# Performance work log

Measured on AMD Instinct MI355X. Metric: run time of the kernel, lower is better.

## Reference

```python
import jax, jax.numpy as jnp
import numpy as np

B, ARITY = 4096, 6
EMB = 100
NF = 200
FC = 1200
N_ROLES, N_VALUES = 5000, 50000
BN_EPS = 1e-5


def setup_inputs() -> dict:
    key = jax.random.key(0)
    ks = jax.random.split(key, 12)
    bound = float(np.sqrt(1.0 / EMB))
    x = jax.random.randint(ks[0], (B, 2 * ARITY), 0, 5000, dtype=jnp.int64)
    emb_roles = jax.random.uniform(ks[1], (N_ROLES, EMB), jnp.float32, -bound, bound)
    emb_values = jax.random.uniform(ks[2], (N_VALUES, EMB), jnp.float32, -bound, bound)
    conv_w = 0.1 * jax.random.normal(ks[3], (NF, 2 * EMB), jnp.float32)  # conv (1,2E) kernel == linear
    conv_b = jnp.zeros((NF,), jnp.float32)
    bn_gamma = jnp.ones((NF,), jnp.float32)
    bn_beta = jnp.zeros((NF,), jnp.float32)
    gW = jax.random.normal(ks[4], (FC, 2 * NF), jnp.float32) * float(np.sqrt(2.0 / (FC + 2 * NF)))
    gb = jnp.zeros((FC,), jnp.float32)
    fW = jax.random.normal(ks[5], (1, FC), jnp.float32) * float(np.sqrt(2.0 / (1 + FC)))
    fb = jnp.zeros((1,), jnp.float32)
    return dict(x=x, emb_roles=emb_roles, emb_values=emb_values, conv_w=conv_w,
                conv_b=conv_b, bn_gamma=bn_gamma, bn_beta=bn_beta,
                gW=gW, gb=gb, fW=fW, fb=fb)


def reference(x, emb_roles, emb_values, conv_w, conv_b, bn_gamma, bn_beta, gW, gb, fW, fb):
    arity = x.shape[1] // 2
    roles = emb_roles[x[:, 0::2]]    # [B, A, E]
    values = emb_values[x[:, 1::2]]  # [B, A, E]
    cat = jnp.concatenate([roles, values], axis=-1)  # [B, A, 2E]
    # conv1 with kernel (1, 2E) == per-row linear 2E -> NF
    m = jnp.einsum('bae,fe->baf', cat, conv_w) + conv_b  # [B, A, NF]
    # BatchNorm2d (training mode: batch statistics over B and A per channel)
    mu = m.mean(axis=(0, 1))
    var = m.var(axis=(0, 1))
    m = (m - mu) * jax.lax.rsqrt(var + BN_EPS) * bn_gamma + bn_beta
    m_rel = jax.nn.relu(m)  # [B, A, NF]
    # all role-value pairs: first tiles the sequence, second repeats each row
    first = jnp.tile(m_rel, (1, arity, 1))           # [B, A*A, NF]
    second = jnp.repeat(m_rel, arity, axis=1)        # [B, A*A, NF]
    pairs = jnp.concatenate([first, second], axis=-1)  # [B, A*A, 2NF]
    g = jax.nn.relu(jnp.einsum('bpf,of->bpo', pairs, gW) + gb)  # [B, A*A, FC]
    min_val = g.min(axis=1)  # [B, FC]
    score = min_val @ fW.T + fb  # [B, 1]
    return score
```

## Files before the change

kernel.cpp:

```cpp
#include <hip/hip_runtime.h>
#include <hip/hip_bf16.h>
#include <hip/hip_fp16.h>

#define B_    4096
#define ARITY 6
#define EMB   100
#define NF    200
#define FC    1200
#define NROWS (B_*ARITY)
#define MPAD  (B_*8)
#define NPAD  2432
#define BN_EPS 1e-5f
#define KP    224
#define SENT  32768.0f
#define NTW   (NPAD/4/16)

typedef _Float16 half8 __attribute__((ext_vector_type(8)));
typedef float f32x4 __attribute__((ext_vector_type(4)));

#define MRAW_OFF 0
#define WH_OFF   2457600
#define WT_OFF   2729984
#define STAT_OFF 2780160

__device__ __forceinline__ void gload16(const void* g, void* l) {
    __builtin_amdgcn_global_load_lds(
        (const __attribute__((address_space(1))) void*)g,
        (__attribute__((address_space(3))) void*)l, 16, 0, 0);
}

__device__ __forceinline__ float4 ld4(const float* rr, const float* vr, int e) {
    if (e < EMB)        return *(const float4*)&rr[e];
    else if (e < 2*EMB) return *(const float4*)&vr[e - EMB];
    float4 z = {0.f,0.f,0.f,0.f}; return z;
}

#define K0_W1 (224*28)
#define K0_W2 (K0_W1 + NPAD*28)
#define K0_W3 (K0_W2 + B_)
#define K0_TOT (K0_W3 + 6400)
__launch_bounds__(256)
__global__ void k0_prep(const float* __restrict__ cw, const float* __restrict__ gW,
                        const float* __restrict__ fb,
                        _Float16* __restrict__ wT,
                        _Float16* __restrict__ W_h, float* __restrict__ out,
                        float* __restrict__ gshad)
{
    int id = blockIdx.x * 256 + threadIdx.x;
    if (id < K0_W1) {
        int f = id / 28, s = id - f*28;
        int ks = s >> 2, ls = s & 3, key = (f >> 1) & 3;
        int off = ks*14336 + f*32 + ((ls ^ key)*8);
        half8 h, l;
        #pragma unroll
        for (int j = 0; j < 8; ++j) {
            int k = s*8 + j;
            float v = (f < NF && k < NF) ? cw[f*NF + k] : 0.f;
            _Float16 hi = (_Float16)v;
            h[j] = hi; l[j] = (_Float16)(v - (float)hi);
        }
        *(half8*)&wT[off] = h;
        *(half8*)&wT[off + 7168] = l;
    } else if (id < K0_W2) {
        int id2 = id - K0_W1;
        int n = id2 / 28, s = id2 - n*28;
        int o = n >> 1, hf = n & 1;
        int off = (n >> 4)*3584 + (s >> 2)*512 + (n & 15)*32 + (s & 3)*8;
        half8 h;
        #pragma unroll
        for (int j = 0; j < 8; ++j) {
            int k = s*8 + j;
            float v = 0.f;
            if (k < NF && n < 2*FC) v = gW[(size_t)o*400 + hf*200 + k];
            if (k == NF) v = SENT;
            h[j] = (_Float16)v;
        }
        *(half8*)&W_h[off] = h;
    } else if (id < K0_W3) {
        out[id - K0_W2] = fb[0];
    } else if (id < K0_TOT) {
        gshad[id - K0_W3] = 0.f;
    }
}

__launch_bounds__(256)
__global__ void k1_mfma(const int* __restrict__ x,
                        const float* __restrict__ er,
                        const float* __restrict__ ev,
                        const _Float16* __restrict__ wT,
                        const float* __restrict__ cb,
                        _Float16* __restrict__ m_raw,
                        float* __restrict__ gshad)
{
    __shared__ __align__(16) char smem[59200];
    float* s_sum = (float*)(smem + 57344);
    float* s_sq  = (float*)(smem + 58144);
    int*   s_ri  = (int*)(smem + 58944);
    int*   s_vi  = (int*)(smem + 59072);

    const int t = threadIdx.x, lane = t & 63, wave = t >> 6;
    const int wm = wave >> 1, wn = wave & 1;
    const int R0 = blockIdx.x * 32;
    const int q = lane >> 4, cx = lane & 15;
    const int rdsw = (q ^ ((cx >> 1) & 3)) * 8;

    if (t < 32) {
        int R = R0 + t, b = R / ARITY, a = R - b * ARITY;
        bool is64 = ((x[1] | x[3] | x[5] | x[7]) == 0);
        int base = b * (2*ARITY) + 2*a;
        s_ri[t] = is64 ? x[2*base]     : x[base];
        s_vi[t] = is64 ? x[2*base + 2] : x[base + 1];
    }
    if (t < NF) { s_sum[t] = 0.f; s_sq[t] = 0.f; }
    __syncthreads();

    {
        _Float16* s_ahi = (_Float16*)smem;
        _Float16* s_alo = s_ahi + 7168;
        for (int c = t; c < 896; c += 256) {
            int row = c / 28, s = c - row*28;
            int key = (row >> 1) & 3;
            int col = (s >> 2)*32 + ((s & 3) ^ key)*8;
            const float* rr = er + (size_t)s_ri[row] * EMB;
            const float* vr = ev + (size_t)s_vi[row] * EMB;
            int e0 = s*8;
            float4 v0 = ld4(rr, vr, e0);
            float4 v1 = ld4(rr, vr, e0 + 4);
            half8 hi, lo;
            hi[0]=(_Float16)v0.x; lo[0]=(_Float16)(v0.x-(float)hi[0]);
            hi[1]=(_Float16)v0.y; lo[1]=(_Float16)(v0.y-(float)hi[1]);
            hi[2]=(_Float16)v0.z; lo[2]=(_Float16)(v0.z-(float)hi[2]);
            hi[3]=(_Float16)v0.w; lo[3]=(_Float16)(v0.w-(float)hi[3]);
            hi[4]=(_Float16)v1.x; lo[4]=(_Float16)(v1.x-(float)hi[4]);
            hi[5]=(_Float16)v1.y; lo[5]=(_Float16)(v1.y-(float)hi[5]);
            hi[6]=(_Float16)v1.z; lo[6]=(_Float16)(v1.z-(float)hi[6]);
            hi[7]=(_Float16)v1.w; lo[7]=(_Float16)(v1.w-(float)hi[7]);
            *(half8*)&s_ahi[row*KP + col] = hi;
            *(half8*)&s_alo[row*KP + col] = lo;
        }
    }
    __syncthreads();

    f32x4 ah[7], al[7];
    {
        const _Float16* s_ahi = (const _Float16*)smem;
        const _Float16* s_alo = s_ahi + 7168;
        int arow = wm*16 + cx;
        #pragma unroll
        for (int ks = 0; ks < 7; ++ks) {
            ah[ks] = *(const f32x4*)&s_ahi[arow*KP + ks*32 + rdsw];
            al[ks] = *(const f32x4*)&s_alo[arow*KP + ks*32 + rdsw];
            asm volatile("" : "+v"(ah[ks]), "+v"(al[ks]));
        }
    }
    __syncthreads();

    #define STAGE_W(KS_, BUF_) do {                                          \
        const char* _src = (const char*)wT + (size_t)(KS_) * 28672;          \
        char* _dst = smem + (BUF_) * 28672;                                  \
        _Pragma("unroll")                                                    \
        for (int _i = 0; _i < 7; ++_i) {                                     \
            int _j = wave + 4*_i;                                            \
            gload16(_src + (size_t)(_j*64 + lane)*16, _dst + _j*1024);       \
        }                                                                    \
    } while (0)

    STAGE_W(0, 0);
    STAGE_W(1, 1);

    f32x4 acc[7];
    #pragma unroll
    for (int nf = 0; nf < 7; ++nf) acc[nf] = (f32x4){0.f,0.f,0.f,0.f};

    for (int ks = 0; ks < 7; ++ks) {
        if (ks < 6) asm volatile("s_waitcnt vmcnt(7)" ::: "memory");
        else        asm volatile("s_waitcnt vmcnt(0)" ::: "memory");
        __builtin_amdgcn_s_barrier();
        __builtin_amdgcn_sched_barrier(0);

        const _Float16* wb = (const _Float16*)(smem + (ks & 1) * 28672);
        #pragma unroll
        for (int nf = 0; nf < 7; ++nf) {
            int rb = (wn*112 + nf*16 + cx)*32 + rdsw;
            half8 bh = *(const half8*)&wb[rb];
            half8 bl = *(const half8*)&wb[7168 + rb];
            acc[nf] = __builtin_amdgcn_mfma_f32_16x16x32_f16(
                __builtin_bit_cast(half8, ah[ks]), bh, acc[nf], 0,0,0);
            acc[nf] = __builtin_amdgcn_mfma_f32_16x16x32_f16(
                __builtin_bit_cast(half8, ah[ks]), bl, acc[nf], 0,0,0);
            acc[nf] = __builtin_amdgcn_mfma_f32_16x16x32_f16(
                __builtin_bit_cast(half8, al[ks]), bh, acc[nf], 0,0,0);
        }
        asm volatile("s_waitcnt lgkmcnt(0)" ::: "memory");
        __builtin_amdgcn_sched_barrier(0);
        __builtin_amdgcn_s_barrier();
        __builtin_amdgcn_sched_barrier(0);
        if (ks + 2 < 7) STAGE_W(ks + 2, ks & 1);
    }

    #pragma unroll
    for (int nf = 0; nf < 7; ++nf) {
        int f = wn*112 + nf*16 + cx;
        bool valid = (f < NF);
        float bias = valid ? cb[f] : 0.f;
        float ps = 0.f, pq = 0.f;
        #pragma unroll
        for (int reg = 0; reg < 4; ++reg) {
            float vv = acc[nf][reg] + bias;
            if (valid) {
                int R = R0 + wm*16 + q*4 + reg;
                m_raw[(size_t)R*NF + f] = (_Float16)vv;
                ps += vv; pq += vv*vv;
            }
        }
        ps += __shfl_xor(ps, 16); ps += __shfl_xor(ps, 32);
        pq += __shfl_xor(pq, 16); pq += __shfl_xor(pq, 32);
        if (valid && q == 0) { atomicAdd(&s_sum[f], ps); atomicAdd(&s_sq[f], pq); }
    }
    __syncthreads();
    if (t < NF) {
        float* g = gshad + (blockIdx.x & 15) * 400;
        atomicAdd(&g[t], s_sum[t]);
        atomicAdd(&g[t + 200], s_sq[t]);
    }
}

__launch_bounds__(256, 2)
__global__ void k3_mfma(const _Float16* __restrict__ m_raw,
                        const float* __restrict__ gshad,
                        const float* __restrict__ gamma,
                        const float* __restrict__ beta,
                        const _Float16* __restrict__ W_h,
                        const float* __restrict__ gb,
                        const float* __restrict__ fW,
                        float* __restrict__ out)
{
    __shared__ __align__(16) char smem[40192];
    float2* gbfw2 = (float2*)(smem + 28672);
    float*  scsh  = (float*)(smem + 28672 + 9728);

    const int t = threadIdx.x, lane = t & 63, wave = t >> 6;
    const int q = lane >> 4, cx = lane & 15;
    const int rdsw = (q ^ ((cx >> 1) & 3)) * 8;

    if (t < 224) {
        float sc = 0.f, sh = 0.f;
        if (t < NF) {
            float s = 0.f, qq = 0.f;
            #pragma unroll
            for (int c = 0; c < 16; ++c) { s += gshad[c*400 + t]; qq += gshad[c*400 + 200 + t]; }
            float inv = 1.0f / (float)NROWS;
            float mu  = s * inv;
            float var = qq * inv - mu*mu;
            float rs  = rsqrtf(var + BN_EPS);
            sc = rs * gamma[t];
            sh = beta[t] - mu*sc;
        }
        scsh[t] = sc; scsh[224 + t] = sh;
    }
    for (int i = t; i < 1216; i += 256) {
        float g = (i < FC) ? gb[i] : 0.f;
        float f = (i < FC) ? fW[i] : 0.f;
        gbfw2[i] = make_float2(g, f);
    }
    __syncthreads();

    {
        _Float16* sa = (_Float16*)smem;
        for (int c = t; c < 1792; c += 256) {
            int Rp = c / 28, s = c - Rp*28;
            int a = Rp & 7, b = Rp >> 3;
            int key = (Rp >> 1) & 3;
            int col = (s >> 2)*32 + ((s & 3) ^ key)*8;
            half8 o;
            #pragma unroll
            for (int j = 0; j < 8; ++j) o[j] = (_Float16)0.f;
            if (a < ARITY && s < 25) {
                int R = (blockIdx.x*8 + b)*ARITY + a;
                half8 in = *(const half8*)&m_raw[(size_t)R*NF + s*8];
                #pragma unroll
                for (int j = 0; j < 8; ++j) {
                    int k = s*8 + j;
                    o[j] = (_Float16)fmaxf((float)in[j]*scsh[k] + scsh[224+k], 0.f);
                }
            } else if (a >= ARITY && s == 25) {
                o[0] = (_Float16)1.0f;
            }
            *(half8*)&sa[Rp*KP + col] = o;
        }
    }
    __syncthreads();

    f32x4 av[4][7];
    {
        const _Float16* sa = (const _Float16*)smem;
        #pragma unroll
        for (int mf = 0; mf < 4; ++mf) {
            int row = mf*16 + cx;
            #pragma unroll
            for (int ks = 0; ks < 7; ++ks)
                av[mf][ks] = *(const f32x4*)&sa[row*KP + ks*32 + rdsw];
        }
    }

    const int nbase = wave * (NPAD/4);
    const char* wsrc = (const char*)W_h + (size_t)nbase * 448;
    const int boff = cx*64 + q*16;

    #define LOADT(BV_, NT_) do {                                             \
        const char* _b = wsrc + (size_t)(NT_)*7168 + boff;                   \
        _Pragma("unroll")                                                    \
        for (int _k = 0; _k < 7; ++_k)                                       \
            BV_[_k] = *(const f32x4*)(_b + _k*1024);                         \
    } while (0)

    #define MFMAT(BV_, ACC_) do {                                            \
        _Pragma("unroll")                                                    \
        for (int _m = 0; _m < 4; ++_m) ACC_[_m] = (f32x4){0.f,0.f,0.f,0.f};  \
        _Pragma("unroll")                                                    \
        for (int _k = 0; _k < 7; ++_k) {                                     \
            _Pragma("unroll")                                                \
            for (int _m = 0; _m < 4; ++_m)                                   \
                ACC_[_m] = __builtin_amdgcn_mfma_f32_16x16x32_f16(           \
                    __builtin_bit_cast(half8, av[_m][_k]),                   \
                    __builtin_bit_cast(half8, BV_[_k]), ACC_[_m], 0, 0, 0);  \
        }                                                                    \
    } while (0)

    float preg[4] = {0.f, 0.f, 0.f, 0.f};

    #define EPI(ACC_, NT_) do {                                              \
        float2 _gf = gbfw2[(nbase + (NT_)*16 + cx) >> 1];                    \
        _Pragma("unroll")                                                    \
        for (int _m = 0; _m < 4; ++_m) {                                     \
            f32x4 _a4 = ACC_[_m];                                            \
            float _v = fminf(fminf(_a4[0], _a4[1]), fminf(_a4[2], _a4[3]));  \
            _v = fminf(_v, __shfl_xor(_v, 16));         \
            float _vp = _v + __shfl_xor(_v, 1);            \
            float _val = fmaxf(_vp + _gf.x, 0.f) * _gf.y;                    \
            if (((q & 1) == 0) && ((cx & 1) == 0)) preg[_m] += _val;         \
        }                                                                    \
    } while (0)

    f32x4 bv0[7], bv1[7];
    f32x4 acc0[4], acc1[4];

    LOADT(bv0, 0);
    LOADT(bv1, 1);
    MFMAT(bv0, acc0);
    for (int k = 0; k < 17; ++k) {
        int nt = 2*k + 1;
        LOADT(bv0, nt + 1); MFMAT(bv1, acc1); EPI(acc0, nt - 1);
        LOADT(bv1, nt + 2); MFMAT(bv0, acc0); EPI(acc1, nt);
    }
    LOADT(bv0, 36); MFMAT(bv1, acc1); EPI(acc0, 34);
    LOADT(bv1, 37); MFMAT(bv0, acc0); EPI(acc1, 35);
    MFMAT(bv1, acc1); EPI(acc0, 36);
    EPI(acc1, 37);

    #pragma unroll
    for (int mf = 0; mf < 4; ++mf) {
        float v = preg[mf];
        v += __shfl_xor(v, 2);
        v += __shfl_xor(v, 4);
        v += __shfl_xor(v, 8);
        if (cx == 0 && (q & 1) == 0) {
            int bb = blockIdx.x*8 + mf*2 + (q >> 1);
            atomicAdd(&out[bb], v);
        }
    }
}

extern "C" void kernel_launch(void* const* d_in, const int* in_sizes, int n_in,
                              void* d_out, int out_size, void* d_ws, size_t ws_size,
                              hipStream_t stream)
{
    const int*   x   = (const int*)  d_in[0];
    const float* er  = (const float*)d_in[1];
    const float* ev  = (const float*)d_in[2];
    const float* cw  = (const float*)d_in[3];
    const float* cb  = (const float*)d_in[4];
    const float* gam = (const float*)d_in[5];
    const float* bet = (const float*)d_in[6];
    const float* gW  = (const float*)d_in[7];
    const float* gb  = (const float*)d_in[8];
    const float* fW  = (const float*)d_in[9];
    const float* fb  = (const float*)d_in[10];

    float* ws = (float*)d_ws;
    _Float16* m_raw = (_Float16*)(ws + MRAW_OFF);
    _Float16* W_h   = (_Float16*)(ws + WH_OFF);
    _Float16* wT    = (_Float16*)(ws + WT_OFF);
    float* gshad    = ws + STAT_OFF;
    float* out      = (float*)d_out;

    k0_prep<<<(K0_TOT + 255)/256, 256, 0, stream>>>(cw, gW, fb, wT, W_h, out, gshad);
    k1_mfma<<<NROWS/32, 256, 0, stream>>>(x, er, ev, wT, cb, m_raw, gshad);
    k3_mfma<<<MPAD/64, 256, 0, stream>>>(m_raw, gshad, gam, bet, W_h, gb, fW, out);
}
```

Before: 73.80 us.

## Pack rows densely in k3 to drop padded arity slots from MFMA tiles

The k3 GEMM previously padded each batch element's 6 rows to 8, giving 64-row tiles with 25% wasted MFMA work. Each block now takes 48 dense rows (8 batch elements × 6) in three 16-row fragments. The epilogue uses lane-selection shuffles to gather per-batch minima that straddle fragment boundaries, which adds more complex index logic and select instructions. The grid is 512 blocks, each with 25% less MFMA work and a smaller A tile in LDS.

Measured after the change: 71.77 us. -2.8%, faster.

```diff
diff --git a/kernel.cpp b/kernel.cpp
--- a/kernel.cpp
+++ b/kernel.cpp
@@ -8,7 +8,6 @@
 #define NF    200
 #define FC    1200
 #define NROWS (B_*ARITY)
-#define MPAD  (B_*8)
 #define NPAD  2432
 #define BN_EPS 1e-5f
 #define KP    224
@@ -235,9 +234,9 @@
                         const float* __restrict__ fW,
                         float* __restrict__ out)
 {
-    __shared__ __align__(16) char smem[40192];
-    float2* gbfw2 = (float2*)(smem + 28672);
-    float*  scsh  = (float*)(smem + 28672 + 9728);
+    __shared__ __align__(16) char smem[33024];
+    float2* gbfw2 = (float2*)(smem + 21504);
+    float*  scsh  = (float*)(smem + 31232);
 
     const int t = threadIdx.x, lane = t & 63, wave = t >> 6;
     const int q = lane >> 4, cx = lane & 15;
@@ -267,35 +266,32 @@
 
     {
         _Float16* sa = (_Float16*)smem;
-        for (int c = t; c < 1792; c += 256) {
-            int Rp = c / 28, s = c - Rp*28;
-            int a = Rp & 7, b = Rp >> 3;
-            int key = (Rp >> 1) & 3;
+        for (int c = t; c < 1344; c += 256) {
+            int row = c / 28, s = c - row*28;
+            int key = (row >> 1) & 3;
             int col = (s >> 2)*32 + ((s & 3) ^ key)*8;
             half8 o;
             #pragma unroll
             for (int j = 0; j < 8; ++j) o[j] = (_Float16)0.f;
-            if (a < ARITY && s < 25) {
-                int R = (blockIdx.x*8 + b)*ARITY + a;
+            if (s < 25) {
+                int R = blockIdx.x*48 + row;
                 half8 in = *(const half8*)&m_raw[(size_t)R*NF + s*8];
                 #pragma unroll
                 for (int j = 0; j < 8; ++j) {
                     int k = s*8 + j;
                     o[j] = (_Float16)fmaxf((float)in[j]*scsh[k] + scsh[224+k], 0.f);
                 }
-            } else if (a >= ARITY && s == 25) {
-                o[0] = (_Float16)1.0f;
             }
-            *(half8*)&sa[Rp*KP + col] = o;
-        }
-    }
-    __syncthreads();
-
-    f32x4 av[4][7];
+            *(half8*)&sa[row*KP + col] = o;
+        }
+    }
+    __syncthreads();
+
+    f32x4 av[3][7];
     {
         const _Float16* sa = (const _Float16*)smem;
         #pragma unroll
-        for (int mf = 0; mf < 4; ++mf) {
+        for (int mf = 0; mf < 3; ++mf) {
             int row = mf*16 + cx;
             #pragma unroll
             for (int ks = 0; ks < 7; ++ks)
@@ -316,34 +312,46 @@
 
     #define MFMAT(BV_, ACC_) do {                                            \
         _Pragma("unroll")                                                    \
-        for (int _m = 0; _m < 4; ++_m) ACC_[_m] = (f32x4){0.f,0.f,0.f,0.f};  \
+        for (int _m = 0; _m < 3; ++_m) ACC_[_m] = (f32x4){0.f,0.f,0.f,0.f};  \
         _Pragma("unroll")                                                    \
         for (int _k = 0; _k < 7; ++_k) {                                     \
             _Pragma("unroll")                                                \
-            for (int _m = 0; _m < 4; ++_m)                                   \
+            for (int _m = 0; _m < 3; ++_m)                                   \
                 ACC_[_m] = __builtin_amdgcn_mfma_f32_16x16x32_f16(           \
                     __builtin_bit_cast(half8, av[_m][_k]),                   \
                     __builtin_bit_cast(half8, BV_[_k]), ACC_[_m], 0, 0, 0);  \
         }                                                                    \
     } while (0)
 
-    float preg[4] = {0.f, 0.f, 0.f, 0.f};
+    float preg16 = 0.f, preg48 = 0.f;
 
     #define EPI(ACC_, NT_) do {                                              \
+        float _h0l = fminf(ACC_[0][0], ACC_[0][1]);                          \
+        float _h0h = fminf(ACC_[0][2], ACC_[0][3]);                          \
+        float _h1l = fminf(ACC_[1][0], ACC_[1][1]);                          \
+        float _h1h = fminf(ACC_[1][2], ACC_[1][3]);                          \
+        float _h2l = fminf(ACC_[2][0], ACC_[2][1]);                          \
+        float _h2h = fminf(ACC_[2][2], ACC_[2][3]);                          \
+        float _f0 = fminf(_h0l, _h0h);                                       \
+        float _f1 = fminf(_h1l, _h1h);                                       \
+        float _f2 = fminf(_h2l, _h2h);                                       \
+        float _u16 = (q==0) ? _h1h : (q==1) ? _h0l : (q==2) ? _h2h : _h1l;   \
+        float _u48 = (q==0) ? _h1l : (q==1) ? _h0h : (q==2) ? _h2l : _h1h;   \
+        float _F16 = (q==0) ? _f0 : (q==3) ? _f2 : _f1;                      \
+        float _F48 = (q<=1) ? _f2 : _f0;                                     \
+        float _v16 = fminf(_F16, __shfl_xor(_u16, 16));                      \
+        float _v48 = fminf(_F48, __shfl_xor(_u48, 48));                      \
+        float _vp16 = _v16 + __shfl_xor(_v16, 1);                            \
+        float _vp48 = _v48 + __shfl_xor(_v48, 1);                            \
         float2 _gf = gbfw2[(nbase + (NT_)*16 + cx) >> 1];                    \
-        _Pragma("unroll")                                                    \
-        for (int _m = 0; _m < 4; ++_m) {                                     \
-            f32x4 _a4 = ACC_[_m];                                            \
-            float _v = fminf(fminf(_a4[0], _a4[1]), fminf(_a4[2], _a4[3]));  \
-            _v = fminf(_v, __shfl_xor(_v, 16));         \
-            float _vp = _v + __shfl_xor(_v, 1);            \
-            float _val = fmaxf(_vp + _gf.x, 0.f) * _gf.y;                    \
-            if (((q & 1) == 0) && ((cx & 1) == 0)) preg[_m] += _val;         \
+        if ((cx & 1) == 0) {                                                 \
+            preg16 += fmaxf(_vp16 + _gf.x, 0.f) * _gf.y;                     \
+            preg48 += fmaxf(_vp48 + _gf.x, 0.f) * _gf.y;                     \
         }                                                                    \
     } while (0)
 
     f32x4 bv0[7], bv1[7];
-    f32x4 acc0[4], acc1[4];
+    f32x4 acc0[3], acc1[3];
 
     LOADT(bv0, 0);
     LOADT(bv1, 1);
@@ -358,16 +366,15 @@
     MFMAT(bv1, acc1); EPI(acc0, 36);
     EPI(acc1, 37);
 
-    #pragma unroll
-    for (int mf = 0; mf < 4; ++mf) {
-        float v = preg[mf];
-        v += __shfl_xor(v, 2);
-        v += __shfl_xor(v, 4);
-        v += __shfl_xor(v, 8);
-        if (cx == 0 && (q & 1) == 0) {
-            int bb = blockIdx.x*8 + mf*2 + (q >> 1);
-            atomicAdd(&out[bb], v);
-        }
+    preg16 += __shfl_xor(preg16, 1); preg16 += __shfl_xor(preg16, 2);
+    preg16 += __shfl_xor(preg16, 4); preg16 += __shfl_xor(preg16, 8);
+    preg48 += __shfl_xor(preg48, 1); preg48 += __shfl_xor(preg48, 2);
+    preg48 += __shfl_xor(preg48, 4); preg48 += __shfl_xor(preg48, 8);
+    if (cx == 0) {
+        int b16 = (q==0) ? 0 : (q==1) ? 3 : (q==2) ? 4 : 7;
+        int b48 = (q==0) ? 5 : (q==1) ? 6 : (q==2) ? 1 : 2;
+        atomicAdd(&out[blockIdx.x*8 + b16], preg16);
+        atomicAdd(&out[blockIdx.x*8 + b48], preg48);
     }
 }
 
@@ -396,5 +403,5 @@
 
     k0_prep<<<(K0_TOT + 255)/256, 256, 0, stream>>>(cw, gW, fb, wT, W_h, out, gshad);
     k1_mfma<<<NROWS/32, 256, 0, stream>>>(x, er, ev, wT, cb, m_raw, gshad);
-    k3_mfma<<<MPAD/64, 256, 0, stream>>>(m_raw, gshad, gam, bet, W_h, gb, fW, out);
-}
+    k3_mfma<<<NROWS/48, 256, 0, stream>>>(m_raw, gshad, gam, bet, W_h, gb, fW, out);
+}
```
